# Performance work log

Hardware: AMD Instinct MI355X
Metric: run time of the kernel (lower is better)

## Reference

```python
import jax, jax.numpy as jnp
import numpy as np

EPS = 1e-5
OFFSET_SCALE = 1.0
KPTS = 9   # 3x3 deformable kernel
GROUP = 1  # in_dim // out_dim


def _bn(x, g, b, m, v):
    # eval-mode BatchNorm2d on (B,C,H,W)
    s = g / jnp.sqrt(v + EPS)
    return x * s[None, :, None, None] + (b - m * s)[None, :, None, None]


def _dcnv4_core(value, offset, mask, offset_scale):
    # value: (B,H,W,G,Cg); offset: (B,H,W,G,K,2) as (dx,dy); mask: (B,H,W,G,K)
    B, H, W, G, Cg = value.shape
    K = mask.shape[-1]
    dt = value.dtype
    ky = jnp.repeat(jnp.arange(3) - 1, 3).astype(dt)
    kx = jnp.tile(jnp.arange(3) - 1, 3).astype(dt)
    grid = jnp.stack([kx, ky], -1)                                   # (K,2)
    base = jnp.stack(jnp.meshgrid(jnp.arange(W, dtype=dt),
                                  jnp.arange(H, dtype=dt),
                                  indexing='xy'), -1)                # (H,W,2) = (x,y)
    loc = base[None, :, :, None, None, :] + (grid + offset) * offset_scale  # (B,H,W,G,K,2)
    px, py = loc[..., 0], loc[..., 1]
    x0 = jnp.floor(px); y0 = jnp.floor(py)
    fx = px - x0; fy = py - y0
    vflat = value.transpose(0, 3, 1, 2, 4).reshape(B, G, H * W, Cg)
    out = jnp.zeros((B, G, H * W, Cg), dt)
    corners = ((0.0, 0.0, (1 - fx) * (1 - fy)), (1.0, 0.0, fx * (1 - fy)),
               (0.0, 1.0, (1 - fx) * fy), (1.0, 1.0, fx * fy))
    for dx, dy, wgt in corners:
        xi = x0 + dx; yi = y0 + dy
        valid = ((xi >= 0) & (xi < W) & (yi >= 0) & (yi < H)).astype(dt)
        idx = (jnp.clip(yi, 0, W and H - 1) * W + jnp.clip(xi, 0, W - 1)).astype(jnp.int32)
        idx = idx.transpose(0, 3, 1, 2, 4).reshape(B, G, H * W * K)
        v = jnp.take_along_axis(vflat, idx[..., None], axis=2).reshape(B, G, H * W, K, Cg)
        w = (wgt * valid * mask).transpose(0, 3, 1, 2, 4).reshape(B, G, H * W, K)
        out = out + jnp.einsum('bgsk,bgskc->bgsc', w, v)
    return out.reshape(B, G, H, W, Cg).transpose(0, 2, 3, 1, 4).reshape(B, H, W, G * Cg)


def setup_inputs() -> dict:
    key = jax.random.key(0)
    B, C, H, W = 8, 128, 64, 64
    C_OUT = 128
    OM = ((GROUP * KPTS * 3 + 7) // 8) * 8  # 32, offset_mask padded width
    ks = jax.random.split(key, 16)
    f = jnp.float32
    sc = 1.0 / np.sqrt(C).astype(np.float32)
    return {
        'x': jax.random.normal(ks[0], (B, C, H, W), f),
        'bn1_g': jax.random.uniform(ks[1], (C,), f, 0.5, 1.5),
        'bn1_b': jax.random.normal(ks[2], (C,), f) * 0.1,
        'bn1_m': jax.random.normal(ks[3], (C,), f) * 0.1,
        'bn1_v': jax.random.uniform(ks[4], (C,), f, 0.5, 1.5),
        'w_pw0': jax.random.normal(ks[5], (C, C), f) * sc,
        'w_vp': jax.random.normal(ks[6], (C, C), f) * sc,
        'b_vp': jnp.zeros((C,), f),
        'w_om': jax.random.normal(ks[7], (C, OM), f) * 0.01,
        'b_om': jnp.zeros((OM,), f),
        'w_op': jax.random.normal(ks[8], (C, C), f) * sc,
        'bn2_g': jax.random.uniform(ks[9], (C,), f, 0.5, 1.5),
        'bn2_b': jax.random.normal(ks[10], (C,), f) * 0.1,
        'bn2_m': jax.random.normal(ks[11], (C,), f) * 0.1,
        'bn2_v': jax.random.uniform(ks[12], (C,), f, 0.5, 1.5),
        'w_pw1': jax.random.normal(ks[13], (C_OUT, C), f) * sc,
    }


def reference(x, bn1_g, bn1_b, bn1_m, bn1_v, w_pw0, w_vp, b_vp, w_om, b_om, w_op,
              bn2_g, bn2_b, bn2_m, bn2_v, w_pw1):
    x = _bn(x, bn1_g, bn1_b, bn1_m, bn1_v)
    x = jnp.einsum('bchw,oc->bohw', x, w_pw0)
    B, C, H, W = x.shape
    x = x.reshape(B, H * W, C)  # raw reshape (faithful to torch .reshape, NOT a permute)
    G, K = GROUP, KPTS
    Cg = C // G
    value = (x @ w_vp + b_vp).reshape(B, H, W, G, Cg)
    om = (x @ w_om + b_om)[..., :G * K * 3].reshape(B, H, W, G, K, 3)
    out = _dcnv4_core(value, om[..., :2], om[..., 2], OFFSET_SCALE)
    out = out.reshape(B, H * W, C) @ w_op
    x = out.reshape(B, C, H, W)  # raw reshape back
    x = _bn(x, bn2_g, bn2_b, bn2_m, bn2_v)
    x = jnp.einsum('bchw,oc->bohw', x, w_pw1)
    return x
```

## Files before the change

kernel.cpp:

```cpp
#include <hip/hip_runtime.h>

#define HW 4096
#define PAD 33
typedef unsigned short ushort;
typedef __attribute__((ext_vector_type(8))) short short8;
typedef __attribute__((ext_vector_type(4))) float f32x4;

__device__ __forceinline__ ushort bf_rne(float f) {
  unsigned u = __float_as_uint(f);
  unsigned r = (u + 0x7fffu + ((u >> 16) & 1u)) >> 16;
  return (ushort)r;
}
__device__ __forceinline__ void split2(float f, ushort& hi, ushort& lo) {
  ushort h = bf_rne(f);
  float hf = __uint_as_float((unsigned)h << 16);
  hi = h;
  lo = bf_rne(f - hf);
}

__global__ __launch_bounds__(256) void prep(
    const float* __restrict__ g1, const float* __restrict__ be1,
    const float* __restrict__ m1, const float* __restrict__ v1,
    const float* __restrict__ w0,
    const float* __restrict__ g2, const float* __restrict__ be2,
    const float* __restrict__ m2, const float* __restrict__ v2,
    const float* __restrict__ w1,
    const float* __restrict__ wvp, const float* __restrict__ wom,
    const float* __restrict__ wop,
    ushort* __restrict__ W0h, ushort* __restrict__ W0l, float* __restrict__ b0,
    ushort* __restrict__ W1h, ushort* __restrict__ W1l, float* __restrict__ b1,
    ushort* __restrict__ vph, ushort* __restrict__ vpl,
    ushort* __restrict__ oph, ushort* __restrict__ opl,
    ushort* __restrict__ omh, ushort* __restrict__ oml)
{
  const int t = threadIdx.x;
  const int role = blockIdx.x;
  if (role < 16) {
    __shared__ float sc[128], sh[128], part[16][17];
    const int cv = role >> 3;
    const float* g  = cv ? g2 : g1;
    const float* be = cv ? be2 : be1;
    const float* mm = cv ? m2 : m1;
    const float* vv = cv ? v2 : v1;
    if (t < 128) {
      float s = g[t] / sqrtf(vv[t] + 1e-5f);
      sc[t] = s;
      sh[t] = be[t] - mm[t] * s;
    }
    __syncthreads();
    const float* ws = cv ? w1 : w0;
    ushort* dh = cv ? W1h : W0h;
    ushort* dl = cv ? W1l : W0l;
    float* bb  = cv ? b1 : b0;
    const int o = ((role & 7) << 4) + (t >> 4);
    const int kl = t & 15;
    float accb = 0.f;
    #pragma unroll
    for (int j = 0; j < 8; ++j) {
      const int k = (kl << 3) + j;
      const float wv = ws[o * 128 + k];
      ushort hi, lo;
      split2(wv * sc[k], hi, lo);
      dh[o * 128 + k] = hi;
      dl[o * 128 + k] = lo;
      accb = fmaf(wv, sh[k], accb);
    }
    part[t >> 4][kl] = accb;
    __syncthreads();
    if (kl == 0) {
      float s = 0.f;
      #pragma unroll
      for (int j = 0; j < 16; ++j) s += part[t >> 4][j];
      bb[o] = s;
    }
  } else if (role < 32) {
    const int rr = role & 7;
    const float* srcM = (role < 24) ? wvp : wop;
    ushort* dh = (role < 24) ? vph : oph;
    ushort* dl = (role < 24) ? vpl : opl;
    const int n = (rr << 4) + (t >> 4);
    const int kl = t & 15;
    #pragma unroll
    for (int j = 0; j < 8; ++j) {
      const int k = (kl << 3) + j;
      ushort hi, lo;
      split2(srcM[k * 128 + n], hi, lo);
      dh[n * 128 + k] = hi;
      dl[n * 128 + k] = lo;
    }
  } else {
    const int n = ((role - 32) << 4) + (t >> 4);
    const int kl = t & 15;
    #pragma unroll
    for (int j = 0; j < 8; ++j) {
      const int k = (kl << 3) + j;
      ushort hi, lo;
      split2(wom[k * 32 + n], hi, lo);
      omh[n * 128 + k] = hi;
      oml[n * 128 + k] = lo;
    }
  }
}

__global__ __launch_bounds__(256) void fused_x_valom(
    const float* __restrict__ x,
    const ushort* __restrict__ W0h, const ushort* __restrict__ W0l,
    const float* __restrict__ b0,
    const ushort* __restrict__ vph, const ushort* __restrict__ vpl,
    const float* __restrict__ bvp, const float* __restrict__ bom,
    float* __restrict__ value, float* __restrict__ omb)
{
  __shared__ __align__(16) char smem[37376];
  __shared__ float b0_s[128], b2_s[160];
  ushort (*Wh_s)[32] = (ushort(*)[32])(smem);
  ushort (*Wl_s)[32] = (ushort(*)[32])(smem + 8192);
  float*  Xf         = (float*)(smem + 16384);
  float*  Yf         = (float*)(smem);
  ushort (*Vh_s)[32] = (ushort(*)[32])(smem + 16896);
  ushort (*Vl_s)[32] = (ushort(*)[32])(smem + 27136);

  const int t = threadIdx.x;
  const int cb = blockIdx.x;
  const int b = blockIdx.y;
  const int hwBase = cb << 7;
  const size_t xbase = (size_t)b * (size_t)(128 * HW);
  if (t < 128) b0_s[t] = b0[t];
  if (t < 160) b2_s[t] = (t < 128) ? bvp[t] : bom[t - 128];
  const int lane = t & 63, w = t >> 6;
  const int col = lane & 15, quad = lane >> 4;
  const int wm1 = (w & 1) << 6, wn1 = (w >> 1) << 6;
  const f32x4 z = {0.f, 0.f, 0.f, 0.f};

  f32x4 acc1[4][4];
  #pragma unroll
  for (int i = 0; i < 4; ++i)
    #pragma unroll
    for (int j = 0; j < 4; ++j) acc1[i][j] = z;

  for (int kc = 0; kc < 4; ++kc) {
    const int kB = kc << 5;
    for (int i = t; i < 512; i += 256) {
      const int o = i >> 2, q8 = (i & 3) << 3;
      *(uint4*)&Wh_s[o][q8] = *(const uint4*)&W0h[o * 128 + kB + q8];
      *(uint4*)&Wl_s[o][q8] = *(const uint4*)&W0l[o * 128 + kB + q8];
    }
    #pragma unroll
    for (int p = 0; p < 4; ++p) {
      const int idx = (p << 8) + t;
      const int c = idx >> 5, j4 = (idx & 31) << 2;
      const float4 f = *(const float4*)&x[xbase + (size_t)(kB + c) * HW + hwBase + j4];
      Xf[(j4 + 0) * PAD + c] = f.x;
      Xf[(j4 + 1) * PAD + c] = f.y;
      Xf[(j4 + 2) * PAD + c] = f.z;
      Xf[(j4 + 3) * PAD + c] = f.w;
    }
    __syncthreads();
    short8 aH[4], aL[4];
    #pragma unroll
    for (int f = 0; f < 4; ++f) {
      const int row = wm1 + (f << 4) + col;
      aH[f] = *(const short8*)&Wh_s[row][quad << 3];
      aL[f] = *(const short8*)&Wl_s[row][quad << 3];
    }
    #pragma unroll
    for (int g = 0; g < 4; ++g) {
      const float* xr = &Xf[(wn1 + (g << 4) + col) * PAD + (quad << 3)];
      union { ushort u[8]; short8 v; } bh, bl;
      #pragma unroll
      for (int j = 0; j < 8; ++j) split2(xr[j], bh.u[j], bl.u[j]);
      #pragma unroll
      for (int f = 0; f < 4; ++f) {
        acc1[f][g] = __builtin_amdgcn_mfma_f32_16x16x32_bf16(aH[f], bh.v, acc1[f][g], 0, 0, 0);
        acc1[f][g] = __builtin_amdgcn_mfma_f32_16x16x32_bf16(aH[f], bl.v, acc1[f][g], 0, 0, 0);
        acc1[f][g] = __builtin_amdgcn_mfma_f32_16x16x32_bf16(aL[f], bh.v, acc1[f][g], 0, 0, 0);
      }
    }
    __syncthreads();
  }

  const int wm2 = (w & 1) << 6;
  const int wn2 = (w >> 1) * 80;
  f32x4 acc2[4][5];
  #pragma unroll
  for (int i = 0; i < 4; ++i)
    #pragma unroll
    for (int j = 0; j < 5; ++j) acc2[i][j] = z;

  for (int j2 = 0; j2 < 4; ++j2) {
    for (int i = t; i < 640; i += 256) {
      const int n = i >> 2, q8 = (i & 3) << 3;
      *(uint4*)&Vh_s[n][q8] = *(const uint4*)&vph[n * 128 + (j2 << 5) + q8];
      *(uint4*)&Vl_s[n][q8] = *(const uint4*)&vpl[n * 128 + (j2 << 5) + q8];
    }
    if ((w >> 1) == (j2 >> 1)) {
      #pragma unroll
      for (int gg = 0; gg < 2; ++gg) {
        const int g = ((j2 & 1) << 1) + gg;
        #pragma unroll
        for (int f = 0; f < 4; ++f) {
          const int o = wm1 + (f << 4) + (quad << 2);
          #pragma unroll
          for (int r = 0; r < 4; ++r)
            Yf[(o + r) * PAD + (gg << 4) + col] = acc1[f][g][r] + b0_s[o + r];
        }
      }
    }
    __syncthreads();
    union { ushort u[8]; short8 v; } a2h[4], a2l[4];
    #pragma unroll
    for (int f2 = 0; f2 < 4; ++f2) {
      const float* yr = &Yf[(wm2 + (f2 << 4) + col) * PAD + (quad << 3)];
      #pragma unroll
      for (int j = 0; j < 8; ++j) split2(yr[j], a2h[f2].u[j], a2l[f2].u[j]);
    }
    #pragma unroll
    for (int g2 = 0; g2 < 5; ++g2) {
      const int n = wn2 + (g2 << 4) + col;
      const short8 vh = *(const short8*)&Vh_s[n][quad << 3];
      const short8 vl = *(const short8*)&Vl_s[n][quad << 3];
      #pragma unroll
      for (int f2 = 0; f2 < 4; ++f2) {
        acc2[f2][g2] = __builtin_amdgcn_mfma_f32_16x16x32_bf16(a2h[f2].v, vh, acc2[f2][g2], 0, 0, 0);
        acc2[f2][g2] = __builtin_amdgcn_mfma_f32_16x16x32_bf16(a2h[f2].v, vl, acc2[f2][g2], 0, 0, 0);
        acc2[f2][g2] = __builtin_amdgcn_mfma_f32_16x16x32_bf16(a2l[f2].v, vh, acc2[f2][g2], 0, 0, 0);
      }
    }
    __syncthreads();
  }
  #pragma unroll
  for (int f2 = 0; f2 < 4; ++f2)
    #pragma unroll
    for (int r = 0; r < 4; ++r) {
      const int m = wm2 + (f2 << 4) + (quad << 2) + r;
      const size_t gRow = (size_t)b * HW + (size_t)m * 32 + cb;
      #pragma unroll
      for (int g2 = 0; g2 < 5; ++g2) {
        const int n = wn2 + (g2 << 4) + col;
        const float v = acc2[f2][g2][r] + b2_s[n];
        if (n < 128) value[gRow * 128 + n] = v;
        else         omb[gRow * 32 + (n - 128)] = v;
      }
    }
}

__global__ __launch_bounds__(256) void dcn_sample(
    const float* __restrict__ value, const float* __restrict__ om,
    ushort* __restrict__ samph, ushort* __restrict__ sampl)
{
  __shared__ float oms[8][32];
  const int t = threadIdx.x;
  const int blk = blockIdx.x;
  const int b = blk >> 9;
  const int sBase = (blk & 511) << 3;
  const int s = sBase + (t >> 5);
  const int cg = (t & 31) << 2;
  oms[t >> 5][t & 31] = om[((size_t)b * HW + sBase + (t >> 5)) * 32 + (t & 31)];
  __syncthreads();
  const int h = s >> 6, wq = s & 63;
  const float* vb = value + (size_t)b * HW * 128;
  const float* omp = oms[t >> 5];
  const float fw = (float)wq, fh = (float)h;
  float4 acc = {0.f, 0.f, 0.f, 0.f};
  #pragma unroll
  for (int k = 0; k < 9; ++k) {
    const float kx = (float)(k % 3 - 1);
    const float ky = (float)(k / 3 - 1);
    const float dx = omp[k * 3 + 0];
    const float dy = omp[k * 3 + 1];
    const float m  = omp[k * 3 + 2];
    const float px = fw + kx + dx;
    const float py = fh + ky + dy;
    const float x0f = floorf(px), y0f = floorf(py);
    const float fx = px - x0f, fy = py - y0f;
    const int ix = (int)x0f, iy = (int)y0f;
    #pragma unroll
    for (int cy = 0; cy < 2; ++cy) {
      const int yi = iy + cy;
      const float wy = cy ? fy : 1.f - fy;
      const float vy = (yi >= 0 && yi < 64) ? 1.f : 0.f;
      const int yc = min(max(yi, 0), 63);
      #pragma unroll
      for (int cx = 0; cx < 2; ++cx) {
        const int xi = ix + cx;
        const float wx = cx ? fx : 1.f - fx;
        const float vx = (xi >= 0 && xi < 64) ? 1.f : 0.f;
        const int xc = min(max(xi, 0), 63);
        const float wgt = wx * wy * vx * vy * m;
        const float4 v = *(const float4*)&vb[(size_t)(yc * 64 + xc) * 128 + cg];
        acc.x = fmaf(wgt, v.x, acc.x);
        acc.y = fmaf(wgt, v.y, acc.y);
        acc.z = fmaf(wgt, v.z, acc.z);
        acc.w = fmaf(wgt, v.w, acc.w);
      }
    }
  }
  ushort h0, l0, h1, l1, h2, l2, h3, l3;
  split2(acc.x, h0, l0); split2(acc.y, h1, l1);
  split2(acc.z, h2, l2); split2(acc.w, h3, l3);
  const size_t idx = ((size_t)b * HW + s) * 128 + cg;
  uint2 uh, ul;
  uh.x = (unsigned)h0 | ((unsigned)h1 << 16);
  uh.y = (unsigned)h2 | ((unsigned)h3 << 16);
  ul.x = (unsigned)l0 | ((unsigned)l1 << 16);
  ul.y = (unsigned)l2 | ((unsigned)l3 << 16);
  *(uint2*)&samph[idx] = uh;
  *(uint2*)&sampl[idx] = ul;
}

__global__ __launch_bounds__(256) void fused_op_out(
    const ushort* __restrict__ samph, const ushort* __restrict__ sampl,
    const ushort* __restrict__ oph, const ushort* __restrict__ opl,
    const ushort* __restrict__ W1h, const ushort* __restrict__ W1l,
    const float* __restrict__ b1, float* __restrict__ out)
{
  __shared__ __align__(16) char smem[33280];
  __shared__ float b1_s[128];
  ushort (*Ah_s)[32]  = (ushort(*)[32])(smem);
  ushort (*Al_s)[32]  = (ushort(*)[32])(smem + 8192);
  ushort (*Bh_s)[32]  = (ushort(*)[32])(smem + 16384);
  ushort (*Bl_s)[32]  = (ushort(*)[32])(smem + 24576);
  float*  Yf          = (float*)(smem);
  ushort (*W1h_s)[32] = (ushort(*)[32])(smem + 16896);
  ushort (*W1l_s)[32] = (ushort(*)[32])(smem + 25088);

  const int t = threadIdx.x;
  const int cb = blockIdx.x;
  const int b = blockIdx.y;
  if (t < 128) b1_s[t] = b1[t];
  const int lane = t & 63, w = t >> 6;
  const int col = lane & 15, quad = lane >> 4;
  const int wm1 = (w & 1) << 6, wn1 = (w >> 1) << 6;
  const f32x4 z = {0.f, 0.f, 0.f, 0.f};

  f32x4 acc1[4][4];
  #pragma unroll
  for (int i = 0; i < 4; ++i)
    #pragma unroll
    for (int j = 0; j < 4; ++j) acc1[i][j] = z;

  for (int kc = 0; kc < 4; ++kc) {
    const int kB = kc << 5;
    for (int i = t; i < 512; i += 256) {
      const int m = i >> 2, q8 = (i & 3) << 3;
      const size_t row = (size_t)b * HW + (size_t)m * 32 + cb;
      *(uint4*)&Ah_s[m][q8] = *(const uint4*)&samph[row * 128 + kB + q8];
      *(uint4*)&Al_s[m][q8] = *(const uint4*)&sampl[row * 128 + kB + q8];
      *(uint4*)&Bh_s[m][q8] = *(const uint4*)&oph[m * 128 + kB + q8];
      *(uint4*)&Bl_s[m][q8] = *(const uint4*)&opl[m * 128 + kB + q8];
    }
    __syncthreads();
    short8 aH[4], aL[4];
    #pragma unroll
    for (int f = 0; f < 4; ++f) {
      const int row = wm1 + (f << 4) + col;
      aH[f] = *(const short8*)&Ah_s[row][quad << 3];
      aL[f] = *(const short8*)&Al_s[row][quad << 3];
    }
    #pragma unroll
    for (int g = 0; g < 4; ++g) {
      const int n = wn1 + (g << 4) + col;
      const short8 bh = *(const short8*)&Bh_s[n][quad << 3];
      const short8 bl = *(const short8*)&Bl_s[n][quad << 3];
      #pragma unroll
      for (int f = 0; f < 4; ++f) {
        acc1[f][g] = __builtin_amdgcn_mfma_f32_16x16x32_bf16(aH[f], bh, acc1[f][g], 0, 0, 0);
        acc1[f][g] = __builtin_amdgcn_mfma_f32_16x16x32_bf16(aH[f], bl, acc1[f][g], 0, 0, 0);
        acc1[f][g] = __builtin_amdgcn_mfma_f32_16x16x32_bf16(aL[f], bh, acc1[f][g], 0, 0, 0);
      }
    }
    __syncthreads();
  }

  const int wm2 = (w & 1) << 6, wn2 = (w >> 1) << 6;
  f32x4 acc2[4][4];
  #pragma unroll
  for (int i = 0; i < 4; ++i)
    #pragma unroll
    for (int j = 0; j < 4; ++j) acc2[i][j] = z;

  for (int j2 = 0; j2 < 4; ++j2) {
    for (int i = t; i < 512; i += 256) {
      const int o = i >> 2, q8 = (i & 3) << 3;
      *(uint4*)&W1h_s[o][q8] = *(const uint4*)&W1h[o * 128 + (j2 << 5) + q8];
      *(uint4*)&W1l_s[o][q8] = *(const uint4*)&W1l[o * 128 + (j2 << 5) + q8];
    }
    if ((w & 1) == (j2 >> 1)) {
      #pragma unroll
      for (int ff = 0; ff < 2; ++ff) {
        const int f = ((j2 & 1) << 1) + ff;
        #pragma unroll
        for (int g = 0; g < 4; ++g) {
          const int j = wn1 + (g << 4) + col;
          #pragma unroll
          for (int r = 0; r < 4; ++r)
            Yf[j * PAD + (ff << 4) + (quad << 2) + r] = acc1[f][g][r];
        }
      }
    }
    __syncthreads();
    union { ushort u[8]; short8 v; } b5h[4], b5l[4];
    #pragma unroll
    for (int g2 = 0; g2 < 4; ++g2) {
      const float* yr = &Yf[(wn2 + (g2 << 4) + col) * PAD + (quad << 3)];
      #pragma unroll
      for (int j = 0; j < 8; ++j) split2(yr[j], b5h[g2].u[j], b5l[g2].u[j]);
    }
    #pragma unroll
    for (int f2 = 0; f2 < 4; ++f2) {
      const int o = wm2 + (f2 << 4) + col;
      const short8 ah = *(const short8*)&W1h_s[o][quad << 3];
      const short8 al = *(const short8*)&W1l_s[o][quad << 3];
      #pragma unroll
      for (int g2 = 0; g2 < 4; ++g2) {
        acc2[f2][g2] = __builtin_amdgcn_mfma_f32_16x16x32_bf16(ah, b5h[g2].v, acc2[f2][g2], 0, 0, 0);
        acc2[f2][g2] = __builtin_amdgcn_mfma_f32_16x16x32_bf16(ah, b5l[g2].v, acc2[f2][g2], 0, 0, 0);
        acc2[f2][g2] = __builtin_amdgcn_mfma_f32_16x16x32_bf16(al, b5h[g2].v, acc2[f2][g2], 0, 0, 0);
      }
    }
    __syncthreads();
  }
  const size_t obase = (size_t)b * (size_t)(128 * HW) + ((size_t)cb << 7);
  #pragma unroll
  for (int f2 = 0; f2 < 4; ++f2)
    #pragma unroll
    for (int r = 0; r < 4; ++r) {
      const int o = wm2 + (f2 << 4) + (quad << 2) + r;
      #pragma unroll
      for (int g2 = 0; g2 < 4; ++g2) {
        const int j = wn2 + (g2 << 4) + col;
        out[obase + (size_t)o * HW + j] = acc2[f2][g2][r] + b1_s[o];
      }
    }
}

extern "C" void kernel_launch(void* const* d_in, const int* in_sizes, int n_in,
                              void* d_out, int out_size, void* d_ws, size_t ws_size,
                              hipStream_t stream)
{
  const float* x    = (const float*)d_in[0];
  const float* g1   = (const float*)d_in[1];
  const float* be1  = (const float*)d_in[2];
  const float* m1   = (const float*)d_in[3];
  const float* v1   = (const float*)d_in[4];
  const float* wpw0 = (const float*)d_in[5];
  const float* wvp  = (const float*)d_in[6];
  const float* bvp  = (const float*)d_in[7];
  const float* womW = (const float*)d_in[8];
  const float* bom  = (const float*)d_in[9];
  const float* wop  = (const float*)d_in[10];
  const float* g2   = (const float*)d_in[11];
  const float* be2  = (const float*)d_in[12];
  const float* m2   = (const float*)d_in[13];
  const float* v2   = (const float*)d_in[14];
  const float* wpw1 = (const float*)d_in[15];

  char* ws = (char*)d_ws;
  float*  value = (float*) (ws + 0);
  float*  omb   = (float*) (ws + 16777216);
  ushort* samph = (ushort*)(ws + 20971520);
  ushort* sampl = (ushort*)(ws + 29360128);
  size_t o = 37748736;
  ushort* W0h = (ushort*)(ws + o); o += 32768;
  ushort* W0l = (ushort*)(ws + o); o += 32768;
  ushort* W1h = (ushort*)(ws + o); o += 32768;
  ushort* W1l = (ushort*)(ws + o); o += 32768;
  ushort* vph = (ushort*)(ws + o); o += 40960;
  ushort* vpl = (ushort*)(ws + o); o += 40960;
  ushort* oph = (ushort*)(ws + o); o += 32768;
  ushort* opl = (ushort*)(ws + o); o += 32768;
  float*  b0  = (float*)(ws + o);  o += 512;
  float*  b1  = (float*)(ws + o);
  ushort* omh = vph + 128 * 128;
  ushort* oml = vpl + 128 * 128;

  prep<<<34, 256, 0, stream>>>(g1, be1, m1, v1, wpw0, g2, be2, m2, v2, wpw1,
                               wvp, womW, wop,
                               W0h, W0l, b0, W1h, W1l, b1,
                               vph, vpl, oph, opl, omh, oml);
  fused_x_valom<<<dim3(32, 8), 256, 0, stream>>>(x, W0h, W0l, b0, vph, vpl,
                                                 bvp, bom, value, omb);
  dcn_sample<<<dim3(4096), 256, 0, stream>>>(value, omb, samph, sampl);
  fused_op_out<<<dim3(32, 8), 256, 0, stream>>>(samph, sampl, oph, opl,
                                                W1h, W1l, b1, (float*)d_out);
}
```

Baseline: 156.0 us.

## Use 512-thread blocks and stage intermediate as pre-split bf16 in LDS

```diff
diff --git a/kernel.cpp b/kernel.cpp
--- a/kernel.cpp
+++ b/kernel.cpp
@@ -1,7 +1,8 @@
 #include <hip/hip_runtime.h>
 
 #define HW 4096
-#define PAD 33
+#define PADF 33
+#define PADU 136
 typedef unsigned short ushort;
 typedef __attribute__((ext_vector_type(8))) short short8;
 typedef __attribute__((ext_vector_type(4))) float f32x4;
@@ -102,7 +103,7 @@
   }
 }
 
-__global__ __launch_bounds__(256) void fused_x_valom(
+__global__ __launch_bounds__(512, 2) void fused_x_valom(
     const float* __restrict__ x,
     const ushort* __restrict__ W0h, const ushort* __restrict__ W0l,
     const float* __restrict__ b0,
@@ -110,14 +111,15 @@
     const float* __restrict__ bvp, const float* __restrict__ bom,
     float* __restrict__ value, float* __restrict__ omb)
 {
-  __shared__ __align__(16) char smem[37376];
+  __shared__ __align__(16) char smem[102912];
   __shared__ float b0_s[128], b2_s[160];
   ushort (*Wh_s)[32] = (ushort(*)[32])(smem);
   ushort (*Wl_s)[32] = (ushort(*)[32])(smem + 8192);
   float*  Xf         = (float*)(smem + 16384);
-  float*  Yf         = (float*)(smem);
-  ushort (*Vh_s)[32] = (ushort(*)[32])(smem + 16896);
-  ushort (*Vl_s)[32] = (ushort(*)[32])(smem + 27136);
+  ushort (*Vh_s)[32] = (ushort(*)[32])(smem);
+  ushort (*Vl_s)[32] = (ushort(*)[32])(smem + 10240);
+  ushort (*Yh)[PADU] = (ushort(*)[PADU])(smem + 33280);
+  ushort (*Yl)[PADU] = (ushort(*)[PADU])(smem + 68096);
 
   const int t = threadIdx.x;
   const int cb = blockIdx.x;
@@ -128,90 +130,81 @@
   if (t < 160) b2_s[t] = (t < 128) ? bvp[t] : bom[t - 128];
   const int lane = t & 63, w = t >> 6;
   const int col = lane & 15, quad = lane >> 4;
-  const int wm1 = (w & 1) << 6, wn1 = (w >> 1) << 6;
   const f32x4 z = {0.f, 0.f, 0.f, 0.f};
 
-  f32x4 acc1[4][4];
-  #pragma unroll
-  for (int i = 0; i < 4; ++i)
-    #pragma unroll
-    for (int j = 0; j < 4; ++j) acc1[i][j] = z;
+  f32x4 acc1[8];
+  #pragma unroll
+  for (int f = 0; f < 8; ++f) acc1[f] = z;
 
   for (int kc = 0; kc < 4; ++kc) {
     const int kB = kc << 5;
-    for (int i = t; i < 512; i += 256) {
-      const int o = i >> 2, q8 = (i & 3) << 3;
+    {
+      const int o = t >> 2, q8 = (t & 3) << 3;
       *(uint4*)&Wh_s[o][q8] = *(const uint4*)&W0h[o * 128 + kB + q8];
       *(uint4*)&Wl_s[o][q8] = *(const uint4*)&W0l[o * 128 + kB + q8];
     }
     #pragma unroll
-    for (int p = 0; p < 4; ++p) {
-      const int idx = (p << 8) + t;
+    for (int p = 0; p < 2; ++p) {
+      const int idx = (p << 9) + t;
       const int c = idx >> 5, j4 = (idx & 31) << 2;
       const float4 f = *(const float4*)&x[xbase + (size_t)(kB + c) * HW + hwBase + j4];
-      Xf[(j4 + 0) * PAD + c] = f.x;
-      Xf[(j4 + 1) * PAD + c] = f.y;
-      Xf[(j4 + 2) * PAD + c] = f.z;
-      Xf[(j4 + 3) * PAD + c] = f.w;
-    }
-    __syncthreads();
-    short8 aH[4], aL[4];
-    #pragma unroll
-    for (int f = 0; f < 4; ++f) {
-      const int row = wm1 + (f << 4) + col;
-      aH[f] = *(const short8*)&Wh_s[row][quad << 3];
-      aL[f] = *(const short8*)&Wl_s[row][quad << 3];
-    }
-    #pragma unroll
-    for (int g = 0; g < 4; ++g) {
-      const float* xr = &Xf[(wn1 + (g << 4) + col) * PAD + (quad << 3)];
-      union { ushort u[8]; short8 v; } bh, bl;
+      Xf[(j4 + 0) * PADF + c] = f.x;
+      Xf[(j4 + 1) * PADF + c] = f.y;
+      Xf[(j4 + 2) * PADF + c] = f.z;
+      Xf[(j4 + 3) * PADF + c] = f.w;
+    }
+    __syncthreads();
+    union { ushort u[8]; short8 v; } bh, bl;
+    {
+      const float* xr = &Xf[((w << 4) + col) * PADF + (quad << 3)];
       #pragma unroll
       for (int j = 0; j < 8; ++j) split2(xr[j], bh.u[j], bl.u[j]);
-      #pragma unroll
-      for (int f = 0; f < 4; ++f) {
-        acc1[f][g] = __builtin_amdgcn_mfma_f32_16x16x32_bf16(aH[f], bh.v, acc1[f][g], 0, 0, 0);
-        acc1[f][g] = __builtin_amdgcn_mfma_f32_16x16x32_bf16(aH[f], bl.v, acc1[f][g], 0, 0, 0);
-        acc1[f][g] = __builtin_amdgcn_mfma_f32_16x16x32_bf16(aL[f], bh.v, acc1[f][g], 0, 0, 0);
-      }
-    }
-    __syncthreads();
-  }
-
-  const int wm2 = (w & 1) << 6;
-  const int wn2 = (w >> 1) * 80;
-  f32x4 acc2[4][5];
-  #pragma unroll
-  for (int i = 0; i < 4; ++i)
+    }
+    #pragma unroll
+    for (int f = 0; f < 8; ++f) {
+      const int row = (f << 4) + col;
+      const short8 aH = *(const short8*)&Wh_s[row][quad << 3];
+      const short8 aL = *(const short8*)&Wl_s[row][quad << 3];
+      acc1[f] = __builtin_amdgcn_mfma_f32_16x16x32_bf16(aH, bh.v, acc1[f], 0, 0, 0);
+      acc1[f] = __builtin_amdgcn_mfma_f32_16x16x32_bf16(aH, bl.v, acc1[f], 0, 0, 0);
+      acc1[f] = __builtin_amdgcn_mfma_f32_16x16x32_bf16(aL, bh.v, acc1[f], 0, 0, 0);
+    }
+    __syncthreads();
+  }
+
+  #pragma unroll
+  for (int f = 0; f < 8; ++f)
+    #pragma unroll
+    for (int r = 0; r < 4; ++r) {
+      const int o = (f << 4) + (quad << 2) + r;
+      const int j = (w << 4) + col;
+      ushort hi, lo;
+      split2(acc1[f][r] + b0_s[o], hi, lo);
+      Yh[o][j] = hi;
+      Yl[o][j] = lo;
+    }
+
+  const int wm2 = (w & 3) << 5;
+  const int wn2 = (w >> 2) * 80;
+  f32x4 acc2[2][5];
+  #pragma unroll
+  for (int i = 0; i < 2; ++i)
     #pragma unroll
     for (int j = 0; j < 5; ++j) acc2[i][j] = z;
 
   for (int j2 = 0; j2 < 4; ++j2) {
-    for (int i = t; i < 640; i += 256) {
+    for (int i = t; i < 640; i += 512) {
       const int n = i >> 2, q8 = (i & 3) << 3;
       *(uint4*)&Vh_s[n][q8] = *(const uint4*)&vph[n * 128 + (j2 << 5) + q8];
       *(uint4*)&Vl_s[n][q8] = *(const uint4*)&vpl[n * 128 + (j2 << 5) + q8];
     }
-    if ((w >> 1) == (j2 >> 1)) {
-      #pragma unroll
-      for (int gg = 0; gg < 2; ++gg) {
-        const int g = ((j2 & 1) << 1) + gg;
-        #pragma unroll
-        for (int f = 0; f < 4; ++f) {
-          const int o = wm1 + (f << 4) + (quad << 2);
-          #pragma unroll
-          for (int r = 0; r < 4; ++r)
-            Yf[(o + r) * PAD + (gg << 4) + col] = acc1[f][g][r] + b0_s[o + r];
-        }
-      }
-    }
-    __syncthreads();
-    union { ushort u[8]; short8 v; } a2h[4], a2l[4];
-    #pragma unroll
-    for (int f2 = 0; f2 < 4; ++f2) {
-      const float* yr = &Yf[(wm2 + (f2 << 4) + col) * PAD + (quad << 3)];
-      #pragma unroll
-      for (int j = 0; j < 8; ++j) split2(yr[j], a2h[f2].u[j], a2l[f2].u[j]);
+    __syncthreads();
+    short8 aH[2], aL[2];
+    #pragma unroll
+    for (int f2 = 0; f2 < 2; ++f2) {
+      const int row = wm2 + (f2 << 4) + col;
+      aH[f2] = *(const short8*)&Yh[row][(j2 << 5) + (quad << 3)];
+      aL[f2] = *(const short8*)&Yl[row][(j2 << 5) + (quad << 3)];
     }
     #pragma unroll
     for (int g2 = 0; g2 < 5; ++g2) {
@@ -219,16 +212,16 @@
       const short8 vh = *(const short8*)&Vh_s[n][quad << 3];
       const short8 vl = *(const short8*)&Vl_s[n][quad << 3];
       #pragma unroll
-      for (int f2 = 0; f2 < 4; ++f2) {
-        acc2[f2][g2] = __builtin_amdgcn_mfma_f32_16x16x32_bf16(a2h[f2].v, vh, acc2[f2][g2], 0, 0, 0);
-        acc2[f2][g2] = __builtin_amdgcn_mfma_f32_16x16x32_bf16(a2h[f2].v, vl, acc2[f2][g2], 0, 0, 0);
-        acc2[f2][g2] = __builtin_amdgcn_mfma_f32_16x16x32_bf16(a2l[f2].v, vh, acc2[f2][g2], 0, 0, 0);
-      }
-    }
-    __syncthreads();
-  }
-  #pragma unroll
-  for (int f2 = 0; f2 < 4; ++f2)
+      for (int f2 = 0; f2 < 2; ++f2) {
+        acc2[f2][g2] = __builtin_amdgcn_mfma_f32_16x16x32_bf16(aH[f2], vh, acc2[f2][g2], 0, 0, 0);
+        acc2[f2][g2] = __builtin_amdgcn_mfma_f32_16x16x32_bf16(aH[f2], vl, acc2[f2][g2], 0, 0, 0);
+        acc2[f2][g2] = __builtin_amdgcn_mfma_f32_16x16x32_bf16(aL[f2], vh, acc2[f2][g2], 0, 0, 0);
+      }
+    }
+    __syncthreads();
+  }
+  #pragma unroll
+  for (int f2 = 0; f2 < 2; ++f2)
     #pragma unroll
     for (int r = 0; r < 4; ++r) {
       const int m = wm2 + (f2 << 4) + (quad << 2) + r;
@@ -250,8 +243,8 @@
   __shared__ float oms[8][32];
   const int t = threadIdx.x;
   const int blk = blockIdx.x;
-  const int b = blk >> 9;
-  const int sBase = (blk & 511) << 3;
+  const int b = blk & 7;
+  const int sBase = (blk >> 3) << 3;
   const int s = sBase + (t >> 5);
   const int cg = (t & 31) << 2;
   oms[t >> 5][t & 31] = om[((size_t)b * HW + sBase + (t >> 5)) * 32 + (t & 31)];
@@ -307,21 +300,22 @@
   *(uint2*)&sampl[idx] = ul;
 }
 
-__global__ __launch_bounds__(256) void fused_op_out(
+__global__ __launch_bounds__(512, 2) void fused_op_out(
     const ushort* __restrict__ samph, const ushort* __restrict__ sampl,
     const ushort* __restrict__ oph, const ushort* __restrict__ opl,
     const ushort* __restrict__ W1h, const ushort* __restrict__ W1l,
     const float* __restrict__ b1, float* __restrict__ out)
 {
-  __shared__ __align__(16) char smem[33280];
+  __shared__ __align__(16) char smem[102400];
   __shared__ float b1_s[128];
   ushort (*Ah_s)[32]  = (ushort(*)[32])(smem);
   ushort (*Al_s)[32]  = (ushort(*)[32])(smem + 8192);
   ushort (*Bh_s)[32]  = (ushort(*)[32])(smem + 16384);
   ushort (*Bl_s)[32]  = (ushort(*)[32])(smem + 24576);
-  float*  Yf          = (float*)(smem);
-  ushort (*W1h_s)[32] = (ushort(*)[32])(smem + 16896);
-  ushort (*W1l_s)[32] = (ushort(*)[32])(smem + 25088);
+  ushort (*W1h_s)[32] = (ushort(*)[32])(smem);
+  ushort (*W1l_s)[32] = (ushort(*)[32])(smem + 8192);
+  ushort (*Yh)[PADU]  = (ushort(*)[PADU])(smem + 32768);
+  ushort (*Yl)[PADU]  = (ushort(*)[PADU])(smem + 67584);
 
   const int t = threadIdx.x;
   const int cb = blockIdx.x;
@@ -329,19 +323,17 @@
   if (t < 128) b1_s[t] = b1[t];
   const int lane = t & 63, w = t >> 6;
   const int col = lane & 15, quad = lane >> 4;
-  const int wm1 = (w & 1) << 6, wn1 = (w >> 1) << 6;
   const f32x4 z = {0.f, 0.f, 0.f, 0.f};
 
-  f32x4 acc1[4][4];
-  #pragma unroll
-  for (int i = 0; i < 4; ++i)
-    #pragma unroll
-    for (int j = 0; j < 4; ++j) acc1[i][j] = z;
+  const int wm1 = (w & 1) << 6, wn1 = (w >> 1) << 5;
+  f32x4 acc1[4][2];
+  #pragma unroll
+  for (int i = 0; i < 4; ++i) { acc1[i][0] = z; acc1[i][1] = z; }
 
   for (int kc = 0; kc < 4; ++kc) {
     const int kB = kc << 5;
-    for (int i = t; i < 512; i += 256) {
-      const int m = i >> 2, q8 = (i & 3) << 3;
+    {
+      const int m = t >> 2, q8 = (t & 3) << 3;
       const size_t row = (size_t)b * HW + (size_t)m * 32 + cb;
       *(uint4*)&Ah_s[m][q8] = *(const uint4*)&samph[row * 128 + kB + q8];
       *(uint4*)&Al_s[m][q8] = *(const uint4*)&sampl[row * 128 + kB + q8];
@@ -357,7 +349,7 @@
       aL[f] = *(const short8*)&Al_s[row][quad << 3];
     }
     #pragma unroll
-    for (int g = 0; g < 4; ++g) {
+    for (int g = 0; g < 2; ++g) {
       const int n = wn1 + (g << 4) + col;
       const short8 bh = *(const short8*)&Bh_s[n][quad << 3];
       const short8 bl = *(const short8*)&Bl_s[n][quad << 3];
@@ -371,50 +363,49 @@
     __syncthreads();
   }
 
-  const int wm2 = (w & 1) << 6, wn2 = (w >> 1) << 6;
-  f32x4 acc2[4][4];
-  #pragma unroll
-  for (int i = 0; i < 4; ++i)
-    #pragma unroll
-    for (int j = 0; j < 4; ++j) acc2[i][j] = z;
+  #pragma unroll
+  for (int f = 0; f < 4; ++f)
+    #pragma unroll
+    for (int g = 0; g < 2; ++g)
+      #pragma unroll
+      for (int r = 0; r < 4; ++r) {
+        const int ch = wm1 + (f << 4) + (quad << 2) + r;
+        const int j  = wn1 + (g << 4) + col;
+        ushort hi, lo;
+        split2(acc1[f][g][r], hi, lo);
+        Yh[j][ch] = hi;
+        Yl[j][ch] = lo;
+      }
+
+  const int wm2 = (w & 1) << 6, wn2 = (w >> 1) << 5;
+  f32x4 acc2[4][2];
+  #pragma unroll
+  for (int i = 0; i < 4; ++i) { acc2[i][0] = z; acc2[i][1] = z; }
 
   for (int j2 = 0; j2 < 4; ++j2) {
-    for (int i = t; i < 512; i += 256) {
-      const int o = i >> 2, q8 = (i & 3) << 3;
+    {
+      const int o = t >> 2, q8 = (t & 3) << 3;
       *(uint4*)&W1h_s[o][q8] = *(const uint4*)&W1h[o * 128 + (j2 << 5) + q8];
       *(uint4*)&W1l_s[o][q8] = *(const uint4*)&W1l[o * 128 + (j2 << 5) + q8];
     }
-    if ((w & 1) == (j2 >> 1)) {
-      #pragma unroll
-      for (int ff = 0; ff < 2; ++ff) {
-        const int f = ((j2 & 1) << 1) + ff;
-        #pragma unroll
-        for (int g = 0; g < 4; ++g) {
-          const int j = wn1 + (g << 4) + col;
-          #pragma unroll
-          for (int r = 0; r < 4; ++r)
-            Yf[j * PAD + (ff << 4) + (quad << 2) + r] = acc1[f][g][r];
-        }
-      }
-    }
-    __syncthreads();
-    union { ushort u[8]; short8 v; } b5h[4], b5l[4];
-    #pragma unroll
-    for (int g2 = 0; g2 < 4; ++g2) {
-      const float* yr = &Yf[(wn2 + (g2 << 4) + col) * PAD + (quad << 3)];
-      #pragma unroll
-      for (int j = 0; j < 8; ++j) split2(yr[j], b5h[g2].u[j], b5l[g2].u[j]);
-    }
+    __syncthreads();
+    short8 aH[4], aL[4];
     #pragma unroll
     for (int f2 = 0; f2 < 4; ++f2) {
-      const int o = wm2 + (f2 << 4) + col;
-      const short8 ah = *(const short8*)&W1h_s[o][quad << 3];
-      const short8 al = *(const short8*)&W1l_s[o][quad << 3];
-      #pragma unroll
-      for (int g2 = 0; g2 < 4; ++g2) {
-        acc2[f2][g2] = __builtin_amdgcn_mfma_f32_16x16x32_bf16(ah, b5h[g2].v, acc2[f2][g2], 0, 0, 0);
-        acc2[f2][g2] = __builtin_amdgcn_mfma_f32_16x16x32_bf16(ah, b5l[g2].v, acc2[f2][g2], 0, 0, 0);
-        acc2[f2][g2] = __builtin_amdgcn_mfma_f32_16x16x32_bf16(al, b5h[g2].v, acc2[f2][g2], 0, 0, 0);
+      const int row = wm2 + (f2 << 4) + col;
+      aH[f2] = *(const short8*)&W1h_s[row][quad << 3];
+      aL[f2] = *(const short8*)&W1l_s[row][quad << 3];
+    }
+    #pragma unroll
+    for (int g2 = 0; g2 < 2; ++g2) {
+      const int j = wn2 + (g2 << 4) + col;
+      const short8 bh = *(const short8*)&Yh[j][(j2 << 5) + (quad << 3)];
+      const short8 bl = *(const short8*)&Yl[j][(j2 << 5) + (quad << 3)];
+      #pragma unroll
+      for (int f2 = 0; f2 < 4; ++f2) {
+        acc2[f2][g2] = __builtin_amdgcn_mfma_f32_16x16x32_bf16(aH[f2], bh, acc2[f2][g2], 0, 0, 0);
+        acc2[f2][g2] = __builtin_amdgcn_mfma_f32_16x16x32_bf16(aH[f2], bl, acc2[f2][g2], 0, 0, 0);
+        acc2[f2][g2] = __builtin_amdgcn_mfma_f32_16x16x32_bf16(aL[f2], bh, acc2[f2][g2], 0, 0, 0);
       }
     }
     __syncthreads();
@@ -426,7 +417,7 @@
     for (int r = 0; r < 4; ++r) {
       const int o = wm2 + (f2 << 4) + (quad << 2) + r;
       #pragma unroll
-      for (int g2 = 0; g2 < 4; ++g2) {
+      for (int g2 = 0; g2 < 2; ++g2) {
         const int j = wn2 + (g2 << 4) + col;
         out[obase + (size_t)o * HW + j] = acc2[f2][g2][r] + b1_s[o];
       }
@@ -477,9 +468,9 @@
                                wvp, womW, wop,
                                W0h, W0l, b0, W1h, W1l, b1,
                                vph, vpl, oph, opl, omh, oml);
-  fused_x_valom<<<dim3(32, 8), 256, 0, stream>>>(x, W0h, W0l, b0, vph, vpl,
+  fused_x_valom<<<dim3(32, 8), 512, 0, stream>>>(x, W0h, W0l, b0, vph, vpl,
                                                  bvp, bom, value, omb);
   dcn_sample<<<dim3(4096), 256, 0, stream>>>(value, omb, samph, sampl);
-  fused_op_out<<<dim3(32, 8), 256, 0, stream>>>(samph, sampl, oph, opl,
+  fused_op_out<<<dim3(32, 8), 512, 0, stream>>>(samph, sampl, oph, opl,
                                                 W1h, W1l, b1, (float*)d_out);
 }
```

After: 148.2 us. 5.0% less time.
